# Performance work log

Hardware: AMD Instinct MI355X
Metric: run time of the kernel (lower is better)

The kernel has to match this reference:

```python
import jax, jax.numpy as jnp
import numpy as np

BATCH, N_GRAPHS, N_NODES, UNITS = 512, 3, 4096, 256

def setup_inputs() -> dict:
    key = jax.random.key(0)
    ks = jax.random.split(key, 11)
    return {
        "inputs": jax.random.normal(ks[0], (BATCH, N_NODES), jnp.float32),
        "state": jax.random.normal(ks[1], (BATCH, UNITS), jnp.float32),
        "adj": jax.random.uniform(ks[2], (N_GRAPHS, N_NODES, N_NODES), jnp.float32),
        "wa": jax.random.uniform(ks[3], (N_GRAPHS,), jnp.float32),
        "w_gcn": jax.random.normal(ks[4], (N_NODES, UNITS), jnp.float32) * (1.0 / np.sqrt(N_NODES)),
        "wz": jax.random.normal(ks[5], (UNITS, UNITS), jnp.float32) * 0.05,
        "uz": jax.random.normal(ks[6], (UNITS, UNITS), jnp.float32) * 0.05,
        "bz": jax.random.normal(ks[7], (UNITS,), jnp.float32) * 0.05,
        "wh": jax.random.normal(ks[8], (UNITS, UNITS), jnp.float32) * 0.05,
        "uh": jax.random.normal(ks[9], (UNITS, UNITS), jnp.float32) * 0.05,
        "bh": jax.random.normal(ks[10], (UNITS,), jnp.float32) * 0.05,
    }

def reference(inputs, state, adj, wa, w_gcn, wz, uz, bz, wh, uh, bh):
    # Weighted sum of the n_graphs adjacency matrices: [g],[g,n,n] -> [n,n]
    adj_mix = jnp.einsum('g,gnm->nm', wa, adj)
    # Graph conv: (inputs @ adj_mix) @ w_gcn, then ReLU -> [batch, units]
    x = jax.nn.relu(jnp.matmul(jnp.matmul(inputs, adj_mix), w_gcn))
    # GRU-style gating
    z = jax.nn.sigmoid(x @ wz + state @ uz + bz)
    h_tilde = jnp.tanh(x @ wh + state @ uh + bh)
    out = (1.0 - z) * state + z * h_tilde
    return out
```

## Files before the change

kernel.cpp:

```cpp
#include <hip/hip_runtime.h>
#include <stdint.h>

typedef _Float16 f16;
typedef __attribute__((ext_vector_type(8))) _Float16 f16x8;
typedef __attribute__((ext_vector_type(4))) float f32x4;

#define NN 4096
#define UN 256

__device__ __forceinline__ f16x8 ld_f16x8(const f16* p){ return *(const f16x8*)p; }
__device__ __forceinline__ f32x4 zero4(){ f32x4 z = {0.f,0.f,0.f,0.f}; return z; }


__global__ __launch_bounds__(256) void kmix(
    const float* __restrict__ adj, const float* __restrict__ wa,
    f16* __restrict__ mixh, f16* __restrict__ mixl)
{
  const float wa0 = wa[0], wa1 = wa[1], wa2 = wa[2];
  const size_t gs = (size_t)NN * NN;
  const size_t stride = (size_t)gridDim.x * 256 * 4;
  for (size_t i = ((size_t)blockIdx.x * 256 + threadIdx.x) * 4; i < gs; i += stride){
    f32x4 a0 = *(const f32x4*)(adj + i);
    f32x4 a1 = *(const f32x4*)(adj + gs + i);
    f32x4 a2 = *(const f32x4*)(adj + 2*gs + i);
    f16 h4[4], l4[4];
    #pragma unroll
    for (int j = 0; j < 4; j++){
      float v = wa0*a0[j] + wa1*a1[j] + wa2*a2[j];
      f16 hh = (f16)v;
      h4[j] = hh; l4[j] = (f16)(v - (float)hh);
    }
    *(uint2*)(mixh + i) = *(const uint2*)h4;
    *(uint2*)(mixl + i) = *(const uint2*)l4;
  }
}

__global__ __launch_bounds__(256) void k0_prep(
    const float* __restrict__ wg, const float* __restrict__ wz,
    const float* __restrict__ uz, const float* __restrict__ wh,
    const float* __restrict__ uh,
    f16* __restrict__ wgB,
    f16* __restrict__ czB_h, f16* __restrict__ czB_l,
    f16* __restrict__ chB_h, f16* __restrict__ chB_l)
{
  __shared__ float lsA[32*256];
  __shared__ float lsB[32*256];
  const int t = threadIdx.x;
  const int b = blockIdx.x;
  if (b < 128){
    const int kcg = b;
    #pragma unroll 8
    for (int i = 0; i < 32; i++)
      lsA[i*256 + t] = wg[(size_t)(kcg*32 + i) * UN + t];
    __syncthreads();
    #pragma unroll
    for (int i = 0; i < 4; i++){
      int o = i*256 + t;
      int l = o & 63;
      int n = ((o >> 6) << 4) + (l & 15);
      int kl = (l >> 4) * 8;
      f16 v8[8];
      #pragma unroll
      for (int j = 0; j < 8; j++) v8[j] = (f16)lsA[(kl + j)*256 + n];
      *(uint4*)(wgB + ((size_t)kcg*1024 + o)*8) = *(const uint4*)v8;
    }
  } else {
    const int kcg = b - 128;
    #pragma unroll 8
    for (int i = 0; i < 32; i++){
      int kg = kcg*32 + i;
      lsA[i*256 + t] = (kg < 256) ? wz[(size_t)kg * UN + t]
                                  : uz[(size_t)(kg - 256) * UN + t];
      lsB[i*256 + t] = (kg < 256) ? wh[(size_t)kg * UN + t]
                                  : uh[(size_t)(kg - 256) * UN + t];
    }
    __syncthreads();
    #pragma unroll
    for (int i = 0; i < 4; i++){
      int o = i*256 + t;
      int l = o & 63;
      int n = ((o >> 6) << 4) + (l & 15);
      int kl = (l >> 4) * 8;
      f16 zh[8], zl[8], hh[8], hl[8];
      #pragma unroll
      for (int j = 0; j < 8; j++){
        float vz = lsA[(kl + j)*256 + n];
        float vh = lsB[(kl + j)*256 + n];
        f16 a = (f16)vz; zh[j] = a; zl[j] = (f16)(vz - (float)a);
        f16 c = (f16)vh; hh[j] = c; hl[j] = (f16)(vh - (float)c);
      }
      size_t off = ((size_t)kcg*1024 + o)*8;
      *(uint4*)(czB_h + off) = *(const uint4*)zh;
      *(uint4*)(czB_l + off) = *(const uint4*)zl;
      *(uint4*)(chB_h + off) = *(const uint4*)hh;
      *(uint4*)(chB_l + off) = *(const uint4*)hl;
    }
  }
}

__global__ __launch_bounds__(256) void k1_w2(
    const f16* __restrict__ mixh, const f16* __restrict__ mixl,
    const f16* __restrict__ wgB, float* __restrict__ W2p)
{
  const int t = threadIdx.x, lane = t & 63, wv = t >> 6;
  const int qm = lane & 15, quad = lane >> 4;
  const int mbase = blockIdx.x * 64 + wv * 16;
  const int kbase = blockIdx.y * 512;
  const size_t arow = (size_t)(mbase + qm) * NN + kbase + quad * 8;
  const f16* pah = mixh + arow;
  const f16* pal = mixl + arow;

  f32x4 acc[16];
  #pragma unroll
  for (int i = 0; i < 16; i++) acc[i] = zero4();

  f16x8 ah = ld_f16x8(pah);
  f16x8 al = ld_f16x8(pal);

  for (int step = 0; step < 16; step++){
    const int kc = step * 32;
    const int kcg = (kbase + kc) >> 5;
    const f16* pb = wgB + ((size_t)kcg*1024 + lane)*8;

    f16x8 bf[8];
    #pragma unroll
    for (int i = 0; i < 8; i++) bf[i] = ld_f16x8(pb + i*512);
    f16x8 bg[8];
    #pragma unroll
    for (int i = 0; i < 8; i++) bg[i] = ld_f16x8(pb + (8+i)*512);

    f16x8 ahn = ah, aln = al;
    if (step < 15){
      ahn = ld_f16x8(pah + kc + 32);
      aln = ld_f16x8(pal + kc + 32);
    }

    #pragma unroll
    for (int tn = 0; tn < 8; tn++){
      acc[tn] = __builtin_amdgcn_mfma_f32_16x16x32_f16(ah, bf[tn], acc[tn], 0, 0, 0);
      acc[tn] = __builtin_amdgcn_mfma_f32_16x16x32_f16(al, bf[tn], acc[tn], 0, 0, 0);
    }
    #pragma unroll
    for (int tn = 0; tn < 8; tn++){
      acc[8+tn] = __builtin_amdgcn_mfma_f32_16x16x32_f16(ah, bg[tn], acc[8+tn], 0, 0, 0);
      acc[8+tn] = __builtin_amdgcn_mfma_f32_16x16x32_f16(al, bg[tn], acc[8+tn], 0, 0, 0);
    }

    ah = ahn; al = aln;
  }

  float* wout = W2p + (size_t)blockIdx.y * ((size_t)NN * UN);
  #pragma unroll
  for (int tn = 0; tn < 16; tn++)
    #pragma unroll
    for (int r = 0; r < 4; r++)
      wout[(size_t)(mbase + quad*4 + r)*UN + tn*16 + qm] = acc[tn][r];
}

__global__ __launch_bounds__(256) void k_cvt(
    const float* __restrict__ W2p, f16* __restrict__ W2B)
{
  __shared__ float ls[32*256];
  const int t = threadIdx.x;
  const int kcg = blockIdx.x;
  const int r0 = t >> 6;
  const int c0 = (t & 63) * 4;
  #pragma unroll
  for (int i = 0; i < 8; i++){
    int r = i*4 + r0;
    const float* src = W2p + (size_t)(kcg*32 + r) * UN + c0;
    f32x4 s = zero4();
    #pragma unroll
    for (int p = 0; p < 8; p++)
      s = s + *(const f32x4*)(src + (size_t)p * ((size_t)NN*UN));
    *(f32x4*)(ls + r*256 + c0) = s;
  }
  __syncthreads();
  #pragma unroll
  for (int i = 0; i < 4; i++){
    int o = i*256 + t;
    int l = o & 63;
    int n = ((o >> 6) << 4) + (l & 15);
    int kl = (l >> 4) * 8;
    f16 v8[8];
    #pragma unroll
    for (int j = 0; j < 8; j++) v8[j] = (f16)ls[(kl + j)*256 + n];
    *(uint4*)(W2B + ((size_t)kcg*1024 + o)*8) = *(const uint4*)v8;
  }
}

__global__ __launch_bounds__(256) void k2_x(
    const float* __restrict__ inputs, const f16* __restrict__ W2B,
    float* __restrict__ xgp)
{
  const int t = threadIdx.x, lane = t & 63, wv = t >> 6;
  const int qm = lane & 15, quad = lane >> 4;
  const int m0 = blockIdx.x * 16;
  const int kbase = blockIdx.y * 512;
  const float* pa = inputs + (size_t)(m0 + qm) * NN + kbase + quad * 8;

  f32x4 acc[4] = { zero4(), zero4(), zero4(), zero4() };

  #pragma unroll 4
  for (int kc = 0; kc < 512; kc += 32){
    f32x4 a0 = *(const f32x4*)(pa + kc);
    f32x4 a1 = *(const f32x4*)(pa + kc + 4);
    const int kcg = (kbase + kc) >> 5;
    const f16* pb = W2B + (((size_t)kcg*16 + wv*4)*64 + lane)*8;
    f16x8 bfr[4];
    #pragma unroll
    for (int tn = 0; tn < 4; tn++) bfr[tn] = ld_f16x8(pb + tn*512);
    f16x8 ah, al;
    #pragma unroll
    for (int j = 0; j < 4; j++){
      f16 h0 = (f16)a0[j], h1 = (f16)a1[j];
      ah[j] = h0;   al[j] = (f16)(a0[j] - (float)h0);
      ah[4+j] = h1; al[4+j] = (f16)(a1[j] - (float)h1);
    }
    #pragma unroll
    for (int tn = 0; tn < 4; tn++){
      acc[tn] = __builtin_amdgcn_mfma_f32_16x16x32_f16(ah, bfr[tn], acc[tn], 0, 0, 0);
      acc[tn] = __builtin_amdgcn_mfma_f32_16x16x32_f16(al, bfr[tn], acc[tn], 0, 0, 0);
    }
  }
  float* xo = xgp + (size_t)blockIdx.y * ((size_t)512 * UN);
  #pragma unroll
  for (int tn = 0; tn < 4; tn++)
    #pragma unroll
    for (int r = 0; r < 4; r++)
      xo[(size_t)(m0 + quad*4 + r)*UN + (wv*4 + tn)*16 + qm] = acc[tn][r];
}

__global__ __launch_bounds__(256) void k_tail(
    const float* __restrict__ xgp, const float* __restrict__ state,
    const f16* __restrict__ czB_h, const f16* __restrict__ czB_l,
    const f16* __restrict__ chB_h, const f16* __restrict__ chB_l,
    const float* __restrict__ bz, const float* __restrict__ bh,
    float* __restrict__ out)
{
  __shared__ f16 xah[16][520];
  __shared__ f16 xal[16][520];
  const int t = threadIdx.x;
  const int m0 = blockIdx.x * 16;

  {
    const int r = t >> 4, cb = (t & 15) * 16;
    #pragma unroll
    for (int cc = 0; cc < 16; cc += 4){
      const int c = cb + cc;
      const float* src = xgp + (size_t)(m0 + r) * UN + c;
      f32x4 s = zero4();
      #pragma unroll
      for (int p = 0; p < 8; p++)
        s = s + *(const f32x4*)(src + (size_t)p * (512*UN));
      f16 h4[4], l4[4];
      #pragma unroll
      for (int j = 0; j < 4; j++){
        float v = fmaxf(s[j], 0.f);
        f16 hh = (f16)v; h4[j] = hh; l4[j] = (f16)(v - (float)hh);
      }
      *(uint2*)&xah[r][c] = *(const uint2*)h4;
      *(uint2*)&xal[r][c] = *(const uint2*)l4;
      f32x4 st = *(const f32x4*)(state + (size_t)(m0 + r) * UN + c);
      #pragma unroll
      for (int j = 0; j < 4; j++){
        f16 hh = (f16)st[j]; h4[j] = hh; l4[j] = (f16)(st[j] - (float)hh);
      }
      *(uint2*)&xah[r][256 + c] = *(const uint2*)h4;
      *(uint2*)&xal[r][256 + c] = *(const uint2*)l4;
    }
  }
  __syncthreads();

  const int lane = t & 63, wv = t >> 6;
  const int qm = lane & 15, quad = lane >> 4;
  f32x4 az[4] = { zero4(), zero4(), zero4(), zero4() };
  f32x4 ag[4] = { zero4(), zero4(), zero4(), zero4() };

  for (int kb = 0; kb < 512; kb += 32){
    f16x8 ah = *(const f16x8*)&xah[qm][kb + quad*8];
    f16x8 al = *(const f16x8*)&xal[qm][kb + quad*8];
    const int kcg = kb >> 5;
    const size_t base = (((size_t)kcg*16 + wv*4)*64 + lane)*8;
    #pragma unroll
    for (int tn = 0; tn < 4; tn++){
      f16x8 bzh = ld_f16x8(czB_h + base + tn*512);
      f16x8 bzl = ld_f16x8(czB_l + base + tn*512);
      f16x8 bhh = ld_f16x8(chB_h + base + tn*512);
      f16x8 bhl = ld_f16x8(chB_l + base + tn*512);
      az[tn] = __builtin_amdgcn_mfma_f32_16x16x32_f16(ah, bzh, az[tn], 0, 0, 0);
      az[tn] = __builtin_amdgcn_mfma_f32_16x16x32_f16(al, bzh, az[tn], 0, 0, 0);
      az[tn] = __builtin_amdgcn_mfma_f32_16x16x32_f16(ah, bzl, az[tn], 0, 0, 0);
      ag[tn] = __builtin_amdgcn_mfma_f32_16x16x32_f16(ah, bhh, ag[tn], 0, 0, 0);
      ag[tn] = __builtin_amdgcn_mfma_f32_16x16x32_f16(al, bhh, ag[tn], 0, 0, 0);
      ag[tn] = __builtin_amdgcn_mfma_f32_16x16x32_f16(ah, bhl, ag[tn], 0, 0, 0);
    }
  }

  #pragma unroll
  for (int tn = 0; tn < 4; tn++){
    const int col = (wv*4 + tn)*16 + qm;
    const float bzv = bz[col], bhv = bh[col];
    #pragma unroll
    for (int r = 0; r < 4; r++){
      const int row = m0 + quad*4 + r;
      const float s = state[(size_t)row*UN + col];
      float z = 1.f / (1.f + __expf(-(az[tn][r] + bzv)));
      float ex = __expf(2.f * (ag[tn][r] + bhv));
      float hh = 1.f - 2.f / (ex + 1.f);
      out[(size_t)row*UN + col] = (1.f - z) * s + z * hh;
    }
  }
}

extern "C" void kernel_launch(void* const* d_in, const int* in_sizes, int n_in,
                              void* d_out, int out_size, void* d_ws, size_t ws_size,
                              hipStream_t stream)
{
  const float* inputs = (const float*)d_in[0];
  const float* state  = (const float*)d_in[1];
  const float* adj    = (const float*)d_in[2];
  const float* wa     = (const float*)d_in[3];
  const float* wg     = (const float*)d_in[4];
  const float* wz     = (const float*)d_in[5];
  const float* uz     = (const float*)d_in[6];
  const float* bz     = (const float*)d_in[7];
  const float* wh     = (const float*)d_in[8];
  const float* uh     = (const float*)d_in[9];
  const float* bh     = (const float*)d_in[10];
  float* out = (float*)d_out;

  char* ws = (char*)d_ws;
  f16* mixh    = (f16*)(ws);
  f16* mixl    = (f16*)(ws + (32u<<20));
  float* W2p   = (float*)(ws + (64u<<20));
  float* xgp   = (float*)(ws + (96u<<20));
  f16* wgB     = (f16*)(ws + (100u<<20));
  f16* W2B     = (f16*)(ws + (102u<<20));
  f16* czB_h   = (f16*)(ws + (104u<<20));
  f16* czB_l   = (f16*)(ws + (104u<<20) + (256u<<10));
  f16* chB_h   = (f16*)(ws + (104u<<20) + (512u<<10));
  f16* chB_l   = (f16*)(ws + (104u<<20) + (768u<<10));

  kmix<<<2048, 256, 0, stream>>>(adj, wa, mixh, mixl);
  k0_prep<<<144, 256, 0, stream>>>(wg, wz, uz, wh, uh,
                                   wgB, czB_h, czB_l, chB_h, chB_l);
  k1_w2<<<dim3(64, 8), 256, 0, stream>>>(mixh, mixl, wgB, W2p);
  k_cvt<<<128, 256, 0, stream>>>(W2p, W2B);
  k2_x<<<dim3(32, 8), 256, 0, stream>>>(inputs, W2B, xgp);
  k_tail<<<32, 256, 0, stream>>>(xgp, state, czB_h, czB_l, chB_h, chB_l,
                                 bz, bh, out);
}
```

Before: 417.9 us.

## Fuse adjacency mixing and fp16 hi/lo split into the W2 GEMM kernel

Removes the separate kmix kernel, which read the three fp32 adjacency matrices and wrote mixed fp16 hi/lo copies to workspace. k1_w2 now loads the three fp32 adjacency tiles directly, forms the weighted sum, and splits it into hi/lo fp16 in registers before the MFMAs. This eliminates a 64MB round trip through global memory and one launch. Each A fragment now costs three fp32 loads instead of two fp16 loads, and more registers are live, which may lower occupancy.

Measured after the change: 377.9 us. 1.11x faster.

```diff
diff --git a/kernel.cpp b/kernel.cpp
--- a/kernel.cpp
+++ b/kernel.cpp
@@ -11,29 +11,6 @@
 __device__ __forceinline__ f16x8 ld_f16x8(const f16* p){ return *(const f16x8*)p; }
 __device__ __forceinline__ f32x4 zero4(){ f32x4 z = {0.f,0.f,0.f,0.f}; return z; }
 
-
-__global__ __launch_bounds__(256) void kmix(
-    const float* __restrict__ adj, const float* __restrict__ wa,
-    f16* __restrict__ mixh, f16* __restrict__ mixl)
-{
-  const float wa0 = wa[0], wa1 = wa[1], wa2 = wa[2];
-  const size_t gs = (size_t)NN * NN;
-  const size_t stride = (size_t)gridDim.x * 256 * 4;
-  for (size_t i = ((size_t)blockIdx.x * 256 + threadIdx.x) * 4; i < gs; i += stride){
-    f32x4 a0 = *(const f32x4*)(adj + i);
-    f32x4 a1 = *(const f32x4*)(adj + gs + i);
-    f32x4 a2 = *(const f32x4*)(adj + 2*gs + i);
-    f16 h4[4], l4[4];
-    #pragma unroll
-    for (int j = 0; j < 4; j++){
-      float v = wa0*a0[j] + wa1*a1[j] + wa2*a2[j];
-      f16 hh = (f16)v;
-      h4[j] = hh; l4[j] = (f16)(v - (float)hh);
-    }
-    *(uint2*)(mixh + i) = *(const uint2*)h4;
-    *(uint2*)(mixl + i) = *(const uint2*)l4;
-  }
-}
 
 __global__ __launch_bounds__(256) void k0_prep(
     const float* __restrict__ wg, const float* __restrict__ wz,
@@ -99,23 +76,27 @@
 }
 
 __global__ __launch_bounds__(256) void k1_w2(
-    const f16* __restrict__ mixh, const f16* __restrict__ mixl,
+    const float* __restrict__ adj, const float* __restrict__ wa,
     const f16* __restrict__ wgB, float* __restrict__ W2p)
 {
   const int t = threadIdx.x, lane = t & 63, wv = t >> 6;
   const int qm = lane & 15, quad = lane >> 4;
   const int mbase = blockIdx.x * 64 + wv * 16;
   const int kbase = blockIdx.y * 512;
-  const size_t arow = (size_t)(mbase + qm) * NN + kbase + quad * 8;
-  const f16* pah = mixh + arow;
-  const f16* pal = mixl + arow;
+  const float wa0 = wa[0], wa1 = wa[1], wa2 = wa[2];
+  const size_t gs = (size_t)NN * NN;
+  const float* pa = adj + (size_t)(mbase + qm) * NN + kbase + quad * 8;
 
   f32x4 acc[16];
   #pragma unroll
   for (int i = 0; i < 16; i++) acc[i] = zero4();
 
-  f16x8 ah = ld_f16x8(pah);
-  f16x8 al = ld_f16x8(pal);
+  f32x4 g[6];
+  #pragma unroll
+  for (int r = 0; r < 2; r++)
+    #pragma unroll
+    for (int gi = 0; gi < 3; gi++)
+      g[gi*2 + r] = *(const f32x4*)(pa + (size_t)gi*gs + r*4);
 
   for (int step = 0; step < 16; step++){
     const int kc = step * 32;
@@ -125,15 +106,30 @@
     f16x8 bf[8];
     #pragma unroll
     for (int i = 0; i < 8; i++) bf[i] = ld_f16x8(pb + i*512);
+
+    f16x8 ah, al;
+    #pragma unroll
+    for (int j = 0; j < 4; j++){
+      float v0 = wa0*g[0][j] + wa1*g[2][j] + wa2*g[4][j];
+      float v1 = wa0*g[1][j] + wa1*g[3][j] + wa2*g[5][j];
+      f16 h0 = (f16)v0, h1 = (f16)v1;
+      ah[j] = h0;   al[j] = (f16)(v0 - (float)h0);
+      ah[4+j] = h1; al[4+j] = (f16)(v1 - (float)h1);
+    }
+
+    f32x4 gn[6];
+    if (step < 15){
+      const float* pan = pa + kc + 32;
+      #pragma unroll
+      for (int r = 0; r < 2; r++)
+        #pragma unroll
+        for (int gi = 0; gi < 3; gi++)
+          gn[gi*2 + r] = *(const f32x4*)(pan + (size_t)gi*gs + r*4);
+    }
+
     f16x8 bg[8];
     #pragma unroll
     for (int i = 0; i < 8; i++) bg[i] = ld_f16x8(pb + (8+i)*512);
-
-    f16x8 ahn = ah, aln = al;
-    if (step < 15){
-      ahn = ld_f16x8(pah + kc + 32);
-      aln = ld_f16x8(pal + kc + 32);
-    }
 
     #pragma unroll
     for (int tn = 0; tn < 8; tn++){
@@ -146,7 +142,8 @@
       acc[8+tn] = __builtin_amdgcn_mfma_f32_16x16x32_f16(al, bg[tn], acc[8+tn], 0, 0, 0);
     }
 
-    ah = ahn; al = aln;
+    #pragma unroll
+    for (int i = 0; i < 6; i++) g[i] = gn[i];
   }
 
   float* wout = W2p + (size_t)blockIdx.y * ((size_t)NN * UN);
@@ -331,21 +328,18 @@
   float* out = (float*)d_out;
 
   char* ws = (char*)d_ws;
-  f16* mixh    = (f16*)(ws);
-  f16* mixl    = (f16*)(ws + (32u<<20));
-  float* W2p   = (float*)(ws + (64u<<20));
-  float* xgp   = (float*)(ws + (96u<<20));
-  f16* wgB     = (f16*)(ws + (100u<<20));
-  f16* W2B     = (f16*)(ws + (102u<<20));
-  f16* czB_h   = (f16*)(ws + (104u<<20));
-  f16* czB_l   = (f16*)(ws + (104u<<20) + (256u<<10));
-  f16* chB_h   = (f16*)(ws + (104u<<20) + (512u<<10));
-  f16* chB_l   = (f16*)(ws + (104u<<20) + (768u<<10));
-
-  kmix<<<2048, 256, 0, stream>>>(adj, wa, mixh, mixl);
+  float* W2p   = (float*)(ws);
+  float* xgp   = (float*)(ws + (32u<<20));
+  f16* wgB     = (f16*)(ws + (36u<<20));
+  f16* W2B     = (f16*)(ws + (38u<<20));
+  f16* czB_h   = (f16*)(ws + (40u<<20));
+  f16* czB_l   = (f16*)(ws + (40u<<20) + (256u<<10));
+  f16* chB_h   = (f16*)(ws + (40u<<20) + (512u<<10));
+  f16* chB_l   = (f16*)(ws + (40u<<20) + (768u<<10));
+
   k0_prep<<<144, 256, 0, stream>>>(wg, wz, uz, wh, uh,
                                    wgB, czB_h, czB_l, chB_h, chB_l);
-  k1_w2<<<dim3(64, 8), 256, 0, stream>>>(mixh, mixl, wgB, W2p);
+  k1_w2<<<dim3(64, 8), 256, 0, stream>>>(adj, wa, wgB, W2p);
   k_cvt<<<128, 256, 0, stream>>>(W2p, W2B);
   k2_x<<<dim3(32, 8), 256, 0, stream>>>(inputs, W2B, xgp);
   k_tail<<<32, 256, 0, stream>>>(xgp, state, czB_h, czB_l, chB_h, chB_l,
```
